# Kernel tuning notes

Hardware: AMD Instinct MI355X
Metric: run time of the kernel (lower is better)

The kernel has to match this reference:

```python
import jax, jax.numpy as jnp
import numpy as np

DIM = 1024
ATT_DIM = 1024
N_HEADS = 16
HEAD_DIM = ATT_DIM // N_HEADS


def q_rsqrt_np(x):
    # Quake fast inverse sqrt with one Newton iteration, as in the source.
    y = np.asarray([x], dtype=np.float32)
    x2 = y * np.float32(0.5)
    i = y.view(np.int32)
    i = np.right_shift(i, 1)
    i = np.int32(1597463007) - i
    y = i.view(np.float32)
    y = y * (np.float32(1.5) - x2 * y * y)
    # module casts to half: self.scaling = q_rsqrt(head_dim).half()
    return float(np.float16(y[0]))

SCALING = q_rsqrt_np(HEAD_DIM)


def own_softmax(x):
    # max in fp32, exp in fp32, cast exp to fp16, sum in fp16, divide -> fp16
    maxes = jnp.max(x, axis=-1, keepdims=True)
    x_exp = jnp.exp(x - maxes).astype(jnp.float16)
    x_exp_sum = jnp.sum(x_exp, axis=-1, keepdims=True)
    return x_exp / x_exp_sum


def setup_inputs() -> dict:
    key = jax.random.key(0)
    k1, k2, k3 = jax.random.split(key, 3)
    tgt_len = 2048
    x = jax.random.normal(k1, (tgt_len, DIM), dtype=jnp.float32)
    # nn.Linear weights: [out_features, in_features]
    W_in = jax.random.normal(k2, (3 * ATT_DIM, DIM), dtype=jnp.float32) * (1.0 / np.sqrt(DIM))
    W_out = jax.random.normal(k3, (DIM, ATT_DIM), dtype=jnp.float32) * (1.0 / np.sqrt(ATT_DIM))
    return {"x": x, "W_in": W_in, "W_out": W_out, "tgt_len": tgt_len}


def reference(x, W_in, W_out, tgt_len):
    qkv = x @ W_in.T  # [N, 3*att_dim]
    q, k, v = jnp.split(qkv, 3, axis=-1)
    # [N, H, D] -> [H, N, D]
    q = q.reshape(tgt_len, N_HEADS, HEAD_DIM).transpose(1, 0, 2)
    k = k.reshape(tgt_len, N_HEADS, HEAD_DIM).transpose(1, 0, 2)
    v = v.reshape(tgt_len, N_HEADS, HEAD_DIM).transpose(1, 0, 2)
    scores = jnp.einsum('hnd,hmd->hnm', q, k) * SCALING  # [H, N, N] fp32
    probs = own_softmax(scores)  # fp16
    ctx = jnp.einsum('hnm,hmd->hnd', probs.astype(jnp.float32), v)  # [H, N, D]
    ctx = ctx.transpose(1, 0, 2).reshape(tgt_len, ATT_DIM)
    return ctx @ W_out.T
```

## Files before the change

kernel.cpp:

```cpp
#include <hip/hip_runtime.h>
#include <cstring>
#include <cstdint>

#define TGT 2048
#define NH 16
#define HD 64
#define DIM 1024
#define OD3 3072

typedef _Float16 f16x8 __attribute__((ext_vector_type(8)));
typedef _Float16 f16x4 __attribute__((ext_vector_type(4)));
typedef _Float16 f16x2 __attribute__((ext_vector_type(2)));
typedef float f32x4 __attribute__((ext_vector_type(4)));
typedef float f32x16 __attribute__((ext_vector_type(16)));

__device__ __forceinline__ void gload16(const void* g, void* l) {
  __builtin_amdgcn_global_load_lds(
      (const __attribute__((address_space(1))) unsigned int*)g,
      (__attribute__((address_space(3))) unsigned int*)l, 16, 0, 0);
}

__global__ void cast_all(const float* __restrict__ x, const float* __restrict__ win,
                         const float* __restrict__ wout, _Float16* __restrict__ xh,
                         _Float16* __restrict__ winh, _Float16* __restrict__ wouth) {
  const int NX = TGT * DIM / 8, NW = OD3 * DIM / 8, NO = DIM * DIM / 8;
  int i = blockIdx.x * blockDim.x + threadIdx.x;
  const float* src;
  _Float16* dst;
  int off;
  if (i < NX) { src = x; dst = xh; off = i; }
  else if (i < NX + NW) { src = win; dst = winh; off = i - NX; }
  else if (i < NX + NW + NO) { src = wout; dst = wouth; off = i - NX - NW; }
  else return;
  const float4* p = (const float4*)(src + (size_t)off * 8);
  float4 a = p[0], b = p[1];
  f16x8 o;
  o[0] = (_Float16)a.x; o[1] = (_Float16)a.y; o[2] = (_Float16)a.z; o[3] = (_Float16)a.w;
  o[4] = (_Float16)b.x; o[5] = (_Float16)b.y; o[6] = (_Float16)b.z; o[7] = (_Float16)b.w;
  *(f16x8*)(dst + (size_t)off * 8) = o;
}

__global__ __launch_bounds__(256) void gemm_qkv(
    const _Float16* __restrict__ A, const _Float16* __restrict__ B,
    _Float16* __restrict__ qh, _Float16* __restrict__ kg, _Float16* __restrict__ vg) {
  __shared__ __attribute__((aligned(16))) _Float16 As[2][4096];
  __shared__ __attribute__((aligned(16))) _Float16 Bs[2][4096];
  const int tid = threadIdx.x, lane = tid & 63, w = tid >> 6;
  const int g = lane >> 4, c = lane & 15;
  const int wr = w >> 1, wc = w & 1;
  const int id = blockIdx.x;
  const int swz = (id & 7) * 48 + (id >> 3);
  const int bm = (swz / 24) * 128, bn = (swz % 24) * 128;
  f32x4 acc[4][4] = {};

#define QKV_STAGE(buf, k0)                                                              \
  {                                                                                     \
    _Pragma("unroll") for (int t = 0; t < 2; ++t) {                                     \
      gload16(A + (size_t)(bm + t * 64 + lane) * DIM + (k0) + w * 8,                    \
              &As[buf][w * 1024 + t * 512]);                                            \
      gload16(B + (size_t)(bn + t * 64 + lane) * DIM + (k0) + w * 8,                    \
              &Bs[buf][w * 1024 + t * 512]);                                            \
    }                                                                                   \
  }

  QKV_STAGE(0, 0);
  __syncthreads();
  for (int kk = 0; kk < 32; ++kk) {
    const int cur = kk & 1;
    if (kk + 1 < 32) QKV_STAGE(cur ^ 1, (kk + 1) * 32);
    f16x8 af[4], bf[4];
#pragma unroll
    for (int m = 0; m < 4; ++m) af[m] = *(const f16x8*)(&As[cur][g * 1024 + (wr * 64 + m * 16 + c) * 8]);
#pragma unroll
    for (int n = 0; n < 4; ++n) bf[n] = *(const f16x8*)(&Bs[cur][g * 1024 + (wc * 64 + n * 16 + c) * 8]);
    __builtin_amdgcn_s_setprio(1);
#pragma unroll
    for (int m = 0; m < 4; ++m)
#pragma unroll
      for (int n = 0; n < 4; ++n)
        acc[m][n] = __builtin_amdgcn_mfma_f32_16x16x32_f16(af[m], bf[n], acc[m][n], 0, 0, 0);
    __builtin_amdgcn_s_setprio(0);
    __syncthreads();
  }
#undef QKV_STAGE

  const int which = bn >> 10;
  const int bnn = bn & 1023;
  if (which == 0) {
#pragma unroll
    for (int m = 0; m < 4; ++m)
#pragma unroll
      for (int n = 0; n < 4; ++n)
#pragma unroll
        for (int j = 0; j < 4; ++j) {
          int row = bm + wr * 64 + m * 16 + g * 4 + j;
          int o = bnn + wc * 64 + n * 16 + c;
          qh[((size_t)(o >> 6) * TGT + row) * HD + (o & 63)] = (_Float16)acc[m][n][j];
        }
  } else if (which == 1) {
#pragma unroll
    for (int m = 0; m < 4; ++m)
#pragma unroll
      for (int n = 0; n < 4; ++n)
#pragma unroll
        for (int j = 0; j < 4; ++j) {
          int krow = bm + wr * 64 + m * 16 + g * 4 + j;
          int o = bnn + wc * 64 + n * 16 + c;
          int hh = o >> 6, d = o & 63;
          int kt = krow >> 7, a = (krow & 127) >> 5, r31 = krow & 31;
          int st = d >> 4, hi2 = (d >> 3) & 1, jd = d & 7;
          kg[(size_t)hh * 131072 + kt * 8192 + ((a * 4 + st) * 64 + hi2 * 32 + r31) * 8 + jd] =
              (_Float16)acc[m][n][j];
        }
  } else {
#pragma unroll
    for (int m = 0; m < 4; ++m)
#pragma unroll
      for (int n = 0; n < 4; ++n) {
        int krow0 = bm + wr * 64 + m * 16 + g * 4;
        int o = bnn + wc * 64 + n * 16 + c;
        int hh = o >> 6, d = o & 63;
        int kt = krow0 >> 7, kr = krow0 & 127;
        int u = kr >> 4, hi2 = (kr >> 3) & 1, jb = kr & 7;
        int e = d >> 5, r31 = d & 31;
        f16x4 v;
#pragma unroll
        for (int j = 0; j < 4; ++j) v[j] = (_Float16)acc[m][n][j];
        *(f16x4*)(vg + (size_t)hh * 131072 + kt * 8192 +
                  ((e * 8 + u) * 64 + hi2 * 32 + r31) * 8 + jb) = v;
      }
  }
}

__global__ __launch_bounds__(256) void gemm_out(
    const _Float16* __restrict__ A, const _Float16* __restrict__ B, float* __restrict__ out) {
  __shared__ __attribute__((aligned(16))) _Float16 As[2][4096];
  __shared__ __attribute__((aligned(16))) _Float16 Bs[2][4096];
  const int tid = threadIdx.x, lane = tid & 63, w = tid >> 6;
  const int g = lane >> 4, c = lane & 15;
  const int wr = w >> 1, wc = w & 1;
  const int id = blockIdx.x;
  const int swz = (id & 7) * 16 + (id >> 3);
  const int bm = (swz / 8) * 128, bn = (swz % 8) * 128;
  f32x4 acc[4][4] = {};

#define OUT_STAGE(buf, k0)                                                              \
  {                                                                                     \
    _Pragma("unroll") for (int t = 0; t < 2; ++t) {                                     \
      gload16(A + (size_t)(bm + t * 64 + lane) * DIM + (k0) + w * 8,                    \
              &As[buf][w * 1024 + t * 512]);                                            \
      gload16(B + (size_t)(bn + t * 64 + lane) * DIM + (k0) + w * 8,                    \
              &Bs[buf][w * 1024 + t * 512]);                                            \
    }                                                                                   \
  }

  OUT_STAGE(0, 0);
  __syncthreads();
  for (int kk = 0; kk < 32; ++kk) {
    const int cur = kk & 1;
    if (kk + 1 < 32) OUT_STAGE(cur ^ 1, (kk + 1) * 32);
    f16x8 af[4], bf[4];
#pragma unroll
    for (int m = 0; m < 4; ++m) af[m] = *(const f16x8*)(&As[cur][g * 1024 + (wr * 64 + m * 16 + c) * 8]);
#pragma unroll
    for (int n = 0; n < 4; ++n) bf[n] = *(const f16x8*)(&Bs[cur][g * 1024 + (wc * 64 + n * 16 + c) * 8]);
    __builtin_amdgcn_s_setprio(1);
#pragma unroll
    for (int m = 0; m < 4; ++m)
#pragma unroll
      for (int n = 0; n < 4; ++n)
        acc[m][n] = __builtin_amdgcn_mfma_f32_16x16x32_f16(af[m], bf[n], acc[m][n], 0, 0, 0);
    __builtin_amdgcn_s_setprio(0);
    __syncthreads();
  }
#undef OUT_STAGE

#pragma unroll
  for (int m = 0; m < 4; ++m)
#pragma unroll
    for (int n = 0; n < 4; ++n)
#pragma unroll
      for (int j = 0; j < 4; ++j) {
        int row = bm + wr * 64 + m * 16 + g * 4 + j;
        int o = bn + wc * 64 + n * 16 + c;
        out[(size_t)row * DIM + o] = acc[m][n][j];
      }
}

__global__ __launch_bounds__(256) void attn(
    const _Float16* __restrict__ qh, const _Float16* __restrict__ kg,
    const _Float16* __restrict__ vg, float* __restrict__ po, float* __restrict__ pml,
    float scal2) {
  __shared__ __attribute__((aligned(16))) _Float16 Ks[2][8192];
  __shared__ __attribute__((aligned(16))) _Float16 Vs[2][8192];
  const int tid = threadIdx.x, lane = tid & 63, w = tid >> 6;
  const int l31 = lane & 31, hi = lane >> 5;
  const int h = blockIdx.y;
  const int qblk = blockIdx.x;
  const int ks = blockIdx.z;
  const int qrow = qblk * 128 + w * 32 + l31;
  const _Float16* kbase = kg + (size_t)h * 131072 + (size_t)ks * 65536;
  const _Float16* vbase = vg + (size_t)h * 131072 + (size_t)ks * 65536;

  f16x8 qf[4];
#pragma unroll
  for (int st = 0; st < 4; ++st)
    qf[st] = *(const f16x8*)(qh + ((size_t)h * TGT + qrow) * HD + st * 16 + hi * 8);

  float m2 = -INFINITY, lsum = 0.f;
  f32x16 o0 = {}, o1 = {};

#define ATTN_STAGE(buf, kt)                                                    \
  {                                                                            \
    _Pragma("unroll") for (int t = 0; t < 4; ++t) {                            \
      int chunk = t * 256 + tid;                                               \
      gload16(kbase + (size_t)(kt) * 8192 + chunk * 8, &Ks[buf][chunk * 8]);   \
      gload16(vbase + (size_t)(kt) * 8192 + chunk * 8, &Vs[buf][chunk * 8]);   \
    }                                                                          \
  }

  ATTN_STAGE(0, 0);
  __syncthreads();

  for (int kt = 0; kt < 8; ++kt) {
    const int cur = kt & 1;
    if (kt + 1 < 8) ATTN_STAGE(cur ^ 1, kt + 1);

    f32x16 sa[4] = {};
    __builtin_amdgcn_s_setprio(1);
#pragma unroll
    for (int a = 0; a < 4; ++a)
#pragma unroll
      for (int st = 0; st < 4; ++st) {
        f16x8 kf = *(const f16x8*)(&Ks[cur][((a * 4 + st) * 64 + lane) * 8]);
        sa[a] = __builtin_amdgcn_mfma_f32_32x32x16_f16(kf, qf[st], sa[a], 0, 0, 0);
      }
    __builtin_amdgcn_s_setprio(0);

    float mx = sa[0][0];
#pragma unroll
    for (int a = 0; a < 4; ++a)
#pragma unroll
      for (int r = 0; r < 16; ++r) mx = fmaxf(mx, sa[a][r]);
    mx = fmaxf(mx, __shfl_xor(mx, 32));
    float pmax = mx * scal2;

    if (!__all(pmax <= m2 + 8.f)) {
      float mnew = fmaxf(m2, pmax);
      float alpha = __builtin_amdgcn_exp2f(m2 - mnew);
      m2 = mnew;
      lsum *= alpha;
#pragma unroll
      for (int r = 0; r < 16; ++r) { o0[r] *= alpha; o1[r] *= alpha; }
    }

    float tsum = 0.f;
#pragma unroll
    for (int a = 0; a < 4; ++a) {
      float p[16];
#pragma unroll
      for (int r = 0; r < 16; ++r)
        p[r] = __builtin_amdgcn_exp2f(__builtin_fmaf(sa[a][r], scal2, -m2));
#pragma unroll
      for (int r = 0; r < 16; ++r) tsum += p[r];
      uint32_t pkL[4][2];
#pragma unroll
      for (int r1 = 0; r1 < 4; ++r1)
#pragma unroll
        for (int pp = 0; pp < 2; ++pp) {
          auto pr = __builtin_amdgcn_cvt_pkrtz(p[4 * r1 + 2 * pp], p[4 * r1 + 2 * pp + 1]);
          memcpy(&pkL[r1][pp], &pr, 4);
        }
#pragma unroll
      for (int ul = 0; ul < 2; ++ul) {
        const int u = 2 * a + ul;
        uint32_t lo0 = pkL[2 * ul][0], lo1 = pkL[2 * ul][1];
        uint32_t hi0 = pkL[2 * ul + 1][0], hi1 = pkL[2 * ul + 1][1];
        uint32_t send0 = hi ? lo0 : hi0, send1 = hi ? lo1 : hi1;
        uint32_t keep0 = hi ? hi0 : lo0, keep1 = hi ? hi1 : lo1;
        uint32_t recv0 = (uint32_t)__shfl_xor((int)send0, 32);
        uint32_t recv1 = (uint32_t)__shfl_xor((int)send1, 32);
        uint32_t fr[4];
        fr[0] = hi ? recv0 : keep0;
        fr[1] = hi ? recv1 : keep1;
        fr[2] = hi ? keep0 : recv0;
        fr[3] = hi ? keep1 : recv1;
        f16x8 pa;
        memcpy(&pa, fr, 16);
        __builtin_amdgcn_s_setprio(1);
        {
          f16x8 v0 = *(const f16x8*)(&Vs[cur][((0 * 8 + u) * 64 + lane) * 8]);
          o0 = __builtin_amdgcn_mfma_f32_32x32x16_f16(v0, pa, o0, 0, 0, 0);
          f16x8 v1 = *(const f16x8*)(&Vs[cur][((1 * 8 + u) * 64 + lane) * 8]);
          o1 = __builtin_amdgcn_mfma_f32_32x32x16_f16(v1, pa, o1, 0, 0, 0);
        }
        __builtin_amdgcn_s_setprio(0);
      }
    }
    tsum += __shfl_xor(tsum, 32);
    lsum += tsum;
    __syncthreads();
  }
#undef ATTN_STAGE

  const size_t pbase = ((((size_t)ks * 16 + h) * 16 + qblk) * 128 + (w * 32 + l31)) * 64;
#pragma unroll
  for (int rq = 0; rq < 4; ++rq) {
    f32x4 va, vb;
#pragma unroll
    for (int j = 0; j < 4; ++j) { va[j] = o0[rq * 4 + j]; vb[j] = o1[rq * 4 + j]; }
    *(f32x4*)(po + pbase + 8 * rq + 4 * hi) = va;
    *(f32x4*)(po + pbase + 32 + 8 * rq + 4 * hi) = vb;
  }
  if (hi == 0) {
    const size_t sbase = ((((size_t)ks * 16 + h) * 16 + qblk) * 128 + (w * 32 + l31)) * 2;
    pml[sbase] = m2;
    pml[sbase + 1] = lsum;
  }
}

__global__ void attn_combine(const float* __restrict__ po, const float* __restrict__ pml,
                             _Float16* __restrict__ ctxh) {
  int i = blockIdx.x * blockDim.x + threadIdx.x;
  int dq = i & 3, hq = i >> 2;
  int h = hq & 15, q = hq >> 4;
  int qblk = q >> 7, qr = q & 127;
  size_t o0b = (((size_t)0 * 16 + h) * 16 + qblk) * 8192 + (size_t)qr * 64 + dq * 16;
  size_t o1b = (((size_t)1 * 16 + h) * 16 + qblk) * 8192 + (size_t)qr * 64 + dq * 16;
  size_t s0 = ((((size_t)0 * 16 + h) * 16 + qblk) * 128 + qr) * 2;
  size_t s1 = ((((size_t)1 * 16 + h) * 16 + qblk) * 128 + qr) * 2;
  float m0 = pml[s0], l0 = pml[s0 + 1];
  float m1 = pml[s1], l1 = pml[s1 + 1];
  float m = fmaxf(m0, m1);
  float e0 = __builtin_amdgcn_exp2f(m0 - m);
  float e1 = __builtin_amdgcn_exp2f(m1 - m);
  float inv = 1.0f / (l0 * e0 + l1 * e1);
  f16x8 out2[2];
#pragma unroll
  for (int t = 0; t < 2; ++t) {
    f32x4 a0 = *(const f32x4*)(po + o0b + t * 8);
    f32x4 a4 = *(const f32x4*)(po + o0b + t * 8 + 4);
    f32x4 b0 = *(const f32x4*)(po + o1b + t * 8);
    f32x4 b4 = *(const f32x4*)(po + o1b + t * 8 + 4);
#pragma unroll
    for (int j = 0; j < 4; ++j) {
      out2[t][j] = (_Float16)((a0[j] * e0 + b0[j] * e1) * inv);
      out2[t][j + 4] = (_Float16)((a4[j] * e0 + b4[j] * e1) * inv);
    }
  }
  _Float16* dst = ctxh + (size_t)q * DIM + h * HD + dq * 16;
  *(f16x8*)(dst) = out2[0];
  *(f16x8*)(dst + 8) = out2[1];
}

static float fp16_round_host(float x) {
  uint32_t u; memcpy(&u, &x, 4);
  uint32_t sign = u & 0x80000000u;
  uint32_t exp = (u >> 23) & 0xff;
  uint32_t m = u & 0x7fffffu;
  uint32_t low = m & 0x1fffu, hi = m >> 13;
  if (low > 0x1000u || (low == 0x1000u && (hi & 1))) hi++;
  if (hi == 0x400u) { hi = 0; exp++; }
  uint32_t r = sign | (exp << 23) | (hi << 13);
  float f; memcpy(&f, &r, 4); return f;
}

extern "C" void kernel_launch(void* const* d_in, const int* in_sizes, int n_in,
                              void* d_out, int out_size, void* d_ws, size_t ws_size,
                              hipStream_t stream) {
  const float* x = (const float*)d_in[0];
  const float* Win = (const float*)d_in[1];
  const float* Wout = (const float*)d_in[2];
  float* out = (float*)d_out;
  char* ws = (char*)d_ws;
  _Float16* xh    = (_Float16*)(ws);
  _Float16* winh  = (_Float16*)(ws + (4ull << 20));
  _Float16* wouth = (_Float16*)(ws + (10ull << 20));
  _Float16* qh    = (_Float16*)(ws + (12ull << 20));
  _Float16* kg    = (_Float16*)(ws + (16ull << 20));
  _Float16* vg    = (_Float16*)(ws + (20ull << 20));
  _Float16* ctxh  = (_Float16*)(ws + (24ull << 20));
  float*    po    = (float*)(ws + (28ull << 20));
  float*    pml   = (float*)(ws + (44ull << 20));

  float y = 64.0f;
  volatile float x2 = 32.0f;
  int ib; memcpy(&ib, &y, 4);
  ib = 1597463007 - (ib >> 1);
  memcpy(&y, &ib, 4);
  volatile float t1 = x2 * y;
  volatile float t2 = t1 * y;
  volatile float t3 = 1.5f - t2;
  y = y * t3;
  const float scaling = fp16_round_host(y);
  const float scal2 = scaling * 1.4426950408889634f;

  const int ncast = (TGT * DIM + OD3 * DIM + DIM * DIM) / 8;
  cast_all<<<(ncast + 255) / 256, 256, 0, stream>>>(x, Win, Wout, xh, winh, wouth);
  gemm_qkv<<<384, 256, 0, stream>>>(xh, winh, qh, kg, vg);
  attn<<<dim3(16, NH, 2), 256, 0, stream>>>(qh, kg, vg, po, pml, scal2);
  attn_combine<<<512, 256, 0, stream>>>(po, pml, ctxh);
  gemm_out<<<128, 256, 0, stream>>>(ctxh, wouth, out);
}
```

Before: 118.5 us.

## Load K/V fragments directly from global memory in attention, dropping LDS staging

The attention kernel no longer stages K and V tiles into double-buffered shared memory with global_load_lds and barriers. Each wave now reads its MFMA fragments straight from global memory (K/V are pre-laid-out in fragment order), which removes the LDS footprint and the per-tile __syncthreads. It also adds a launch-bounds occupancy hint of 3 and switches to a 1D grid whose block index is remapped so that consecutively launched blocks spread across heads, aiming at better L2 reuse. The trade-off is that the four waves of a block now each fetch the same K/V data through the cache hierarchy instead of sharing it once via LDS, and load latency is no longer hidden by explicit prefetching.

```diff
diff --git a/kernel.cpp b/kernel.cpp
--- a/kernel.cpp
+++ b/kernel.cpp
@@ -187,20 +187,19 @@
       }
 }
 
-__global__ __launch_bounds__(256) void attn(
+__global__ __launch_bounds__(256, 3) void attn(
     const _Float16* __restrict__ qh, const _Float16* __restrict__ kg,
     const _Float16* __restrict__ vg, float* __restrict__ po, float* __restrict__ pml,
     float scal2) {
-  __shared__ __attribute__((aligned(16))) _Float16 Ks[2][8192];
-  __shared__ __attribute__((aligned(16))) _Float16 Vs[2][8192];
   const int tid = threadIdx.x, lane = tid & 63, w = tid >> 6;
   const int l31 = lane & 31, hi = lane >> 5;
-  const int h = blockIdx.y;
-  const int qblk = blockIdx.x;
-  const int ks = blockIdx.z;
+  const int id = blockIdx.x;
+  const int h = (id & 7) * 2 + ((id >> 3) & 1);
+  const int idx = id >> 4;
+  const int qblk = idx & 15, ks = idx >> 4;
   const int qrow = qblk * 128 + w * 32 + l31;
-  const _Float16* kbase = kg + (size_t)h * 131072 + (size_t)ks * 65536;
-  const _Float16* vbase = vg + (size_t)h * 131072 + (size_t)ks * 65536;
+  const _Float16* kb = kg + (size_t)h * 131072 + (size_t)ks * 65536;
+  const _Float16* vb = vg + (size_t)h * 131072 + (size_t)ks * 65536;
 
   f16x8 qf[4];
 #pragma unroll
@@ -210,21 +209,9 @@
   float m2 = -INFINITY, lsum = 0.f;
   f32x16 o0 = {}, o1 = {};
 
-#define ATTN_STAGE(buf, kt)                                                    \
-  {                                                                            \
-    _Pragma("unroll") for (int t = 0; t < 4; ++t) {                            \
-      int chunk = t * 256 + tid;                                               \
-      gload16(kbase + (size_t)(kt) * 8192 + chunk * 8, &Ks[buf][chunk * 8]);   \
-      gload16(vbase + (size_t)(kt) * 8192 + chunk * 8, &Vs[buf][chunk * 8]);   \
-    }                                                                          \
-  }
-
-  ATTN_STAGE(0, 0);
-  __syncthreads();
-
   for (int kt = 0; kt < 8; ++kt) {
-    const int cur = kt & 1;
-    if (kt + 1 < 8) ATTN_STAGE(cur ^ 1, kt + 1);
+    const _Float16* kt_k = kb + (size_t)kt * 8192;
+    const _Float16* kt_v = vb + (size_t)kt * 8192;
 
     f32x16 sa[4] = {};
     __builtin_amdgcn_s_setprio(1);
@@ -232,7 +219,7 @@
     for (int a = 0; a < 4; ++a)
 #pragma unroll
       for (int st = 0; st < 4; ++st) {
-        f16x8 kf = *(const f16x8*)(&Ks[cur][((a * 4 + st) * 64 + lane) * 8]);
+        f16x8 kf = *(const f16x8*)(kt_k + ((a * 4 + st) * 64 + lane) * 8);
         sa[a] = __builtin_amdgcn_mfma_f32_32x32x16_f16(kf, qf[st], sa[a], 0, 0, 0);
       }
     __builtin_amdgcn_s_setprio(0);
@@ -289,9 +276,9 @@
         memcpy(&pa, fr, 16);
         __builtin_amdgcn_s_setprio(1);
         {
-          f16x8 v0 = *(const f16x8*)(&Vs[cur][((0 * 8 + u) * 64 + lane) * 8]);
+          f16x8 v0 = *(const f16x8*)(kt_v + ((0 * 8 + u) * 64 + lane) * 8);
           o0 = __builtin_amdgcn_mfma_f32_32x32x16_f16(v0, pa, o0, 0, 0, 0);
-          f16x8 v1 = *(const f16x8*)(&Vs[cur][((1 * 8 + u) * 64 + lane) * 8]);
+          f16x8 v1 = *(const f16x8*)(kt_v + ((1 * 8 + u) * 64 + lane) * 8);
           o1 = __builtin_amdgcn_mfma_f32_32x32x16_f16(v1, pa, o1, 0, 0, 0);
         }
         __builtin_amdgcn_s_setprio(0);
@@ -299,18 +286,16 @@
     }
     tsum += __shfl_xor(tsum, 32);
     lsum += tsum;
-    __syncthreads();
-  }
-#undef ATTN_STAGE
+  }
 
   const size_t pbase = ((((size_t)ks * 16 + h) * 16 + qblk) * 128 + (w * 32 + l31)) * 64;
 #pragma unroll
   for (int rq = 0; rq < 4; ++rq) {
-    f32x4 va, vb;
-#pragma unroll
-    for (int j = 0; j < 4; ++j) { va[j] = o0[rq * 4 + j]; vb[j] = o1[rq * 4 + j]; }
+    f32x4 va, vb2;
+#pragma unroll
+    for (int j = 0; j < 4; ++j) { va[j] = o0[rq * 4 + j]; vb2[j] = o1[rq * 4 + j]; }
     *(f32x4*)(po + pbase + 8 * rq + 4 * hi) = va;
-    *(f32x4*)(po + pbase + 32 + 8 * rq + 4 * hi) = vb;
+    *(f32x4*)(po + pbase + 32 + 8 * rq + 4 * hi) = vb2;
   }
   if (hi == 0) {
     const size_t sbase = ((((size_t)ks * 16 + h) * 16 + qblk) * 128 + (w * 32 + l31)) * 2;
@@ -398,7 +383,7 @@
   const int ncast = (TGT * DIM + OD3 * DIM + DIM * DIM) / 8;
   cast_all<<<(ncast + 255) / 256, 256, 0, stream>>>(x, Win, Wout, xh, winh, wouth);
   gemm_qkv<<<384, 256, 0, stream>>>(xh, winh, qh, kg, vg);
-  attn<<<dim3(16, NH, 2), 256, 0, stream>>>(qh, kg, vg, po, pml, scal2);
+  attn<<<512, 256, 0, stream>>>(qh, kg, vg, po, pml, scal2);
   attn_combine<<<512, 256, 0, stream>>>(po, pml, ctxh);
   gemm_out<<<128, 256, 0, stream>>>(ctxh, wouth, out);
 }
```

Result: slower. 149.7 us (+26.3%).

## Shrink attention KV tile to 64 and split keys four ways

Applied to the files above, without the earlier changes.

The K/V global layout written by the QKV GEMM moves from 128-key tiles to 64-key tiles, and the attention kernel now processes 64 keys per iteration with half-size shared buffers and a launch bound asking for 4 blocks per SM. The key dimension is split into 4 chunks instead of 2 when the workspace is large enough, which doubles the number of attention blocks to improve occupancy and parallelism across CUs. The combine kernel is generalized to merge a variable number of partial results. The cost is more partial-output traffic to write and read back, and more loop iterations each doing less work.

```diff
diff --git a/kernel.cpp b/kernel.cpp
--- a/kernel.cpp
+++ b/kernel.cpp
@@ -107,9 +107,9 @@
           int krow = bm + wr * 64 + m * 16 + g * 4 + j;
           int o = bnn + wc * 64 + n * 16 + c;
           int hh = o >> 6, d = o & 63;
-          int kt = krow >> 7, a = (krow & 127) >> 5, r31 = krow & 31;
+          int kt = krow >> 6, a = (krow >> 5) & 1, r31 = krow & 31;
           int st = d >> 4, hi2 = (d >> 3) & 1, jd = d & 7;
-          kg[(size_t)hh * 131072 + kt * 8192 + ((a * 4 + st) * 64 + hi2 * 32 + r31) * 8 + jd] =
+          kg[(size_t)hh * 131072 + kt * 4096 + ((a * 4 + st) * 64 + hi2 * 32 + r31) * 8 + jd] =
               (_Float16)acc[m][n][j];
         }
   } else {
@@ -120,14 +120,13 @@
         int krow0 = bm + wr * 64 + m * 16 + g * 4;
         int o = bnn + wc * 64 + n * 16 + c;
         int hh = o >> 6, d = o & 63;
-        int kt = krow0 >> 7, kr = krow0 & 127;
-        int u = kr >> 4, hi2 = (kr >> 3) & 1, jb = kr & 7;
+        int kt = krow0 >> 6, u = (krow0 >> 4) & 3, hi2 = (krow0 >> 3) & 1, jb = krow0 & 7;
         int e = d >> 5, r31 = d & 31;
         f16x4 v;
 #pragma unroll
         for (int j = 0; j < 4; ++j) v[j] = (_Float16)acc[m][n][j];
-        *(f16x4*)(vg + (size_t)hh * 131072 + kt * 8192 +
-                  ((e * 8 + u) * 64 + hi2 * 32 + r31) * 8 + jb) = v;
+        *(f16x4*)(vg + (size_t)hh * 131072 + kt * 4096 +
+                  ((e * 4 + u) * 64 + hi2 * 32 + r31) * 8 + jb) = v;
       }
   }
 }
@@ -187,20 +186,19 @@
       }
 }
 
-__global__ __launch_bounds__(256) void attn(
+__global__ __launch_bounds__(256, 4) void attn(
     const _Float16* __restrict__ qh, const _Float16* __restrict__ kg,
     const _Float16* __restrict__ vg, float* __restrict__ po, float* __restrict__ pml,
     float scal2) {
-  __shared__ __attribute__((aligned(16))) _Float16 Ks[2][8192];
-  __shared__ __attribute__((aligned(16))) _Float16 Vs[2][8192];
+  __shared__ __attribute__((aligned(16))) _Float16 Ks[2][4096];
+  __shared__ __attribute__((aligned(16))) _Float16 Vs[2][4096];
   const int tid = threadIdx.x, lane = tid & 63, w = tid >> 6;
   const int l31 = lane & 31, hi = lane >> 5;
-  const int h = blockIdx.y;
-  const int qblk = blockIdx.x;
-  const int ks = blockIdx.z;
+  const int h = blockIdx.y, qblk = blockIdx.x, ks = blockIdx.z;
+  const int ntiles = 32 / gridDim.z;
   const int qrow = qblk * 128 + w * 32 + l31;
-  const _Float16* kbase = kg + (size_t)h * 131072 + (size_t)ks * 65536;
-  const _Float16* vbase = vg + (size_t)h * 131072 + (size_t)ks * 65536;
+  const _Float16* kb = kg + (size_t)h * 131072 + (size_t)ks * ntiles * 4096;
+  const _Float16* vb = vg + (size_t)h * 131072 + (size_t)ks * ntiles * 4096;
 
   f16x8 qf[4];
 #pragma unroll
@@ -212,24 +210,24 @@
 
 #define ATTN_STAGE(buf, kt)                                                    \
   {                                                                            \
-    _Pragma("unroll") for (int t = 0; t < 4; ++t) {                            \
+    _Pragma("unroll") for (int t = 0; t < 2; ++t) {                            \
       int chunk = t * 256 + tid;                                               \
-      gload16(kbase + (size_t)(kt) * 8192 + chunk * 8, &Ks[buf][chunk * 8]);   \
-      gload16(vbase + (size_t)(kt) * 8192 + chunk * 8, &Vs[buf][chunk * 8]);   \
+      gload16(kb + (size_t)(kt) * 4096 + chunk * 8, &Ks[buf][chunk * 8]);      \
+      gload16(vb + (size_t)(kt) * 4096 + chunk * 8, &Vs[buf][chunk * 8]);      \
     }                                                                          \
   }
 
   ATTN_STAGE(0, 0);
   __syncthreads();
 
-  for (int kt = 0; kt < 8; ++kt) {
+  for (int kt = 0; kt < ntiles; ++kt) {
     const int cur = kt & 1;
-    if (kt + 1 < 8) ATTN_STAGE(cur ^ 1, kt + 1);
-
-    f32x16 sa[4] = {};
+    if (kt + 1 < ntiles) ATTN_STAGE(cur ^ 1, kt + 1);
+
+    f32x16 sa[2] = {};
     __builtin_amdgcn_s_setprio(1);
 #pragma unroll
-    for (int a = 0; a < 4; ++a)
+    for (int a = 0; a < 2; ++a)
 #pragma unroll
       for (int st = 0; st < 4; ++st) {
         f16x8 kf = *(const f16x8*)(&Ks[cur][((a * 4 + st) * 64 + lane) * 8]);
@@ -239,7 +237,7 @@
 
     float mx = sa[0][0];
 #pragma unroll
-    for (int a = 0; a < 4; ++a)
+    for (int a = 0; a < 2; ++a)
 #pragma unroll
       for (int r = 0; r < 16; ++r) mx = fmaxf(mx, sa[a][r]);
     mx = fmaxf(mx, __shfl_xor(mx, 32));
@@ -256,7 +254,7 @@
 
     float tsum = 0.f;
 #pragma unroll
-    for (int a = 0; a < 4; ++a) {
+    for (int a = 0; a < 2; ++a) {
       float p[16];
 #pragma unroll
       for (int r = 0; r < 16; ++r)
@@ -289,9 +287,9 @@
         memcpy(&pa, fr, 16);
         __builtin_amdgcn_s_setprio(1);
         {
-          f16x8 v0 = *(const f16x8*)(&Vs[cur][((0 * 8 + u) * 64 + lane) * 8]);
+          f16x8 v0 = *(const f16x8*)(&Vs[cur][((0 * 4 + u) * 64 + lane) * 8]);
           o0 = __builtin_amdgcn_mfma_f32_32x32x16_f16(v0, pa, o0, 0, 0, 0);
-          f16x8 v1 = *(const f16x8*)(&Vs[cur][((1 * 8 + u) * 64 + lane) * 8]);
+          f16x8 v1 = *(const f16x8*)(&Vs[cur][((1 * 4 + u) * 64 + lane) * 8]);
           o1 = __builtin_amdgcn_mfma_f32_32x32x16_f16(v1, pa, o1, 0, 0, 0);
         }
         __builtin_amdgcn_s_setprio(0);
@@ -306,11 +304,11 @@
   const size_t pbase = ((((size_t)ks * 16 + h) * 16 + qblk) * 128 + (w * 32 + l31)) * 64;
 #pragma unroll
   for (int rq = 0; rq < 4; ++rq) {
-    f32x4 va, vb;
-#pragma unroll
-    for (int j = 0; j < 4; ++j) { va[j] = o0[rq * 4 + j]; vb[j] = o1[rq * 4 + j]; }
+    f32x4 va, vb2;
+#pragma unroll
+    for (int j = 0; j < 4; ++j) { va[j] = o0[rq * 4 + j]; vb2[j] = o1[rq * 4 + j]; }
     *(f32x4*)(po + pbase + 8 * rq + 4 * hi) = va;
-    *(f32x4*)(po + pbase + 32 + 8 * rq + 4 * hi) = vb;
+    *(f32x4*)(po + pbase + 32 + 8 * rq + 4 * hi) = vb2;
   }
   if (hi == 0) {
     const size_t sbase = ((((size_t)ks * 16 + h) * 16 + qblk) * 128 + (w * 32 + l31)) * 2;
@@ -320,37 +318,50 @@
 }
 
 __global__ void attn_combine(const float* __restrict__ po, const float* __restrict__ pml,
-                             _Float16* __restrict__ ctxh) {
+                             _Float16* __restrict__ ctxh, int nks) {
   int i = blockIdx.x * blockDim.x + threadIdx.x;
   int dq = i & 3, hq = i >> 2;
   int h = hq & 15, q = hq >> 4;
   int qblk = q >> 7, qr = q & 127;
-  size_t o0b = (((size_t)0 * 16 + h) * 16 + qblk) * 8192 + (size_t)qr * 64 + dq * 16;
-  size_t o1b = (((size_t)1 * 16 + h) * 16 + qblk) * 8192 + (size_t)qr * 64 + dq * 16;
-  size_t s0 = ((((size_t)0 * 16 + h) * 16 + qblk) * 128 + qr) * 2;
-  size_t s1 = ((((size_t)1 * 16 + h) * 16 + qblk) * 128 + qr) * 2;
-  float m0 = pml[s0], l0 = pml[s0 + 1];
-  float m1 = pml[s1], l1 = pml[s1 + 1];
-  float m = fmaxf(m0, m1);
-  float e0 = __builtin_amdgcn_exp2f(m0 - m);
-  float e1 = __builtin_amdgcn_exp2f(m1 - m);
-  float inv = 1.0f / (l0 * e0 + l1 * e1);
-  f16x8 out2[2];
-#pragma unroll
-  for (int t = 0; t < 2; ++t) {
-    f32x4 a0 = *(const f32x4*)(po + o0b + t * 8);
-    f32x4 a4 = *(const f32x4*)(po + o0b + t * 8 + 4);
-    f32x4 b0 = *(const f32x4*)(po + o1b + t * 8);
-    f32x4 b4 = *(const f32x4*)(po + o1b + t * 8 + 4);
-#pragma unroll
-    for (int j = 0; j < 4; ++j) {
-      out2[t][j] = (_Float16)((a0[j] * e0 + b0[j] * e1) * inv);
-      out2[t][j + 4] = (_Float16)((a4[j] * e0 + b4[j] * e1) * inv);
+  float m = -INFINITY;
+#pragma unroll 4
+  for (int ks = 0; ks < 4; ++ks)
+    if (ks < nks) {
+      size_t s = ((((size_t)ks * 16 + h) * 16 + qblk) * 128 + qr) * 2;
+      m = fmaxf(m, pml[s]);
     }
-  }
+  float es[4] = {};
+  float l = 0.f;
+#pragma unroll 4
+  for (int ks = 0; ks < 4; ++ks)
+    if (ks < nks) {
+      size_t s = ((((size_t)ks * 16 + h) * 16 + qblk) * 128 + qr) * 2;
+      float e = __builtin_amdgcn_exp2f(pml[s] - m);
+      es[ks] = e;
+      l += pml[s + 1] * e;
+    }
+  float inv = 1.0f / l;
+  float accv[16] = {};
+#pragma unroll 4
+  for (int ks = 0; ks < 4; ++ks)
+    if (ks < nks) {
+      size_t ob = (((size_t)ks * 16 + h) * 16 + qblk) * 8192 + (size_t)qr * 64 + dq * 16;
+      float e = es[ks];
+#pragma unroll
+      for (int t = 0; t < 4; ++t) {
+        f32x4 a = *(const f32x4*)(po + ob + t * 4);
+#pragma unroll
+        for (int j = 0; j < 4; ++j) accv[t * 4 + j] += a[j] * e;
+      }
+    }
+  f16x8 o2[2];
+#pragma unroll
+  for (int t = 0; t < 2; ++t)
+#pragma unroll
+    for (int j = 0; j < 8; ++j) o2[t][j] = (_Float16)(accv[t * 8 + j] * inv);
   _Float16* dst = ctxh + (size_t)q * DIM + h * HD + dq * 16;
-  *(f16x8*)(dst) = out2[0];
-  *(f16x8*)(dst + 8) = out2[1];
+  *(f16x8*)(dst) = o2[0];
+  *(f16x8*)(dst + 8) = o2[1];
 }
 
 static float fp16_round_host(float x) {
@@ -380,8 +391,9 @@
   _Float16* kg    = (_Float16*)(ws + (16ull << 20));
   _Float16* vg    = (_Float16*)(ws + (20ull << 20));
   _Float16* ctxh  = (_Float16*)(ws + (24ull << 20));
-  float*    po    = (float*)(ws + (28ull << 20));
-  float*    pml   = (float*)(ws + (44ull << 20));
+  const int nks = (ws_size >= (62ull << 20)) ? 4 : 2;
+  float* po  = (float*)(ws + (28ull << 20));
+  float* pml = (float*)(ws + ((28ull + 8ull * (unsigned)nks) << 20));
 
   float y = 64.0f;
   volatile float x2 = 32.0f;
@@ -398,7 +410,7 @@
   const int ncast = (TGT * DIM + OD3 * DIM + DIM * DIM) / 8;
   cast_all<<<(ncast + 255) / 256, 256, 0, stream>>>(x, Win, Wout, xh, winh, wouth);
   gemm_qkv<<<384, 256, 0, stream>>>(xh, winh, qh, kg, vg);
-  attn<<<dim3(16, NH, 2), 256, 0, stream>>>(qh, kg, vg, po, pml, scal2);
-  attn_combine<<<512, 256, 0, stream>>>(po, pml, ctxh);
+  attn<<<dim3(16, NH, nks), 256, 0, stream>>>(qh, kg, vg, po, pml, scal2);
+  attn_combine<<<512, 256, 0, stream>>>(po, pml, ctxh, nks);
   gemm_out<<<128, 256, 0, stream>>>(ctxh, wouth, out);
 }
```

Result: slower. 121.2 us (+2.3%).
